# Performance work log

Hardware: AMD Instinct MI355X
Metric: run time of the kernel (lower is better)

## Reference

```python
import jax, jax.numpy as jnp
import numpy as np

K_TOP = 10
DEPTH = 1
N_RULES = 2
N_HOPS = 2
IS_REVERSED = (False, True)


def setup_inputs() -> dict:
    key = jax.random.key(0)
    ks = jax.random.split(key, 11)
    B, E, N, F = 16, 256, 1024, 2048
    return {
        'rel': jax.random.normal(ks[0], (B, E), jnp.float32),
        'arg1': jax.random.normal(ks[1], (B, E), jnp.float32),
        'arg2': jax.random.normal(ks[2], (B, E), jnp.float32),
        'fact_rel': jax.random.normal(ks[3], (B, F, E), jnp.float32),
        'fact_arg1': jax.random.normal(ks[4], (B, F, E), jnp.float32),
        'fact_arg2': jax.random.normal(ks[5], (B, F, E), jnp.float32),
        'nb_facts': jax.random.randint(ks[6], (B,), 1, F + 1),
        'entity_embeddings': jax.random.normal(ks[7], (B, N, E), jnp.float32),
        'nb_entities': jax.random.randint(ks[8], (B,), 1, N + 1),
        'W': jax.random.normal(ks[9], (N_RULES, N_HOPS, E, E), jnp.float32) / np.sqrt(E),
        'b': jnp.zeros((N_RULES, N_HOPS, E), jnp.float32),
    }


def _kernel_scores(q, f):
    # q: [B, M, E], f: [B, F, E] -> Gaussian kernel exp(-0.5*||q-f||^2): [B, M, F]
    d = (jnp.sum(q * q, -1)[..., None] + jnp.sum(f * f, -1)[:, None, :]
         - 2.0 * jnp.einsum('bme,bfe->bmf', q, f))
    return jnp.exp(-0.5 * jnp.maximum(d, 0.0))


def kb_score(rel, arg1, arg2, fact_rel, fact_arg1, fact_arg2, nb_facts):
    # BatchNeuralKB.score: product of per-component kernels, mask padded facts, max over facts.
    B, F, E = fact_rel.shape
    M = rel.shape[0] // B
    r = rel.reshape(B, M, E); a1 = arg1.reshape(B, M, E); a2 = arg2.reshape(B, M, E)
    s = (_kernel_scores(r, fact_rel) * _kernel_scores(a1, fact_arg1)
         * _kernel_scores(a2, fact_arg2))                       # [B, M, F]
    mask = jnp.arange(F)[None, None, :] < nb_facts[:, None, None]
    s = jnp.where(mask, s, 0.0)
    return jnp.max(s, axis=-1).reshape(-1)                      # [B*M]


def prove(rel, arg1, arg2, fact_rel, fact_arg1, fact_arg2, nb_facts,
          entity_embeddings, W, b, depth):
    scores_0 = kb_score(rel, arg1, arg2, fact_rel, fact_arg1, fact_arg2, nb_facts)
    if depth == 0:
        return scores_0
    B, E = rel.shape
    N = entity_embeddings.shape[1]
    global_res = None
    for rule_idx in range(N_RULES):
        is_rev = IS_REVERSED[rule_idx]
        hop_rel_lst = [rel @ W[rule_idx, h] + b[rule_idx, h] for h in range(N_HOPS)]
        sources, scores = arg1, None
        for hop_idx, hop_rel in enumerate(hop_rel_lst, start=1):
            sources_2d = sources.reshape(-1, E)
            nb_branches = sources_2d.shape[0] // B
            hop_rel_2d = jnp.repeat(hop_rel, nb_branches, axis=0)   # [B*br, E]
            if hop_idx < N_HOPS:
                ent_rep = jnp.repeat(entity_embeddings, nb_branches, axis=0)  # [B*br, N, E]
                all_ent_2d = ent_rep.reshape(-1, E)                  # [B*br*N, E]
                new_src_2d = jnp.repeat(sources_2d, N, axis=0)       # [B*br*N, E]
                hop_rel_big = jnp.repeat(hop_rel_2d, N, axis=0)
                na1, na2 = (all_ent_2d, new_src_2d) if is_rev else (new_src_2d, all_ent_2d)
                new_scores = prove(hop_rel_big, na1, na2, fact_rel, fact_arg1,
                                   fact_arg2, nb_facts, entity_embeddings, W, b,
                                   depth - 1).reshape(-1, N)         # [B*br, N]
                k = min(K_TOP, N)
                z_scores, z_idx = jax.lax.top_k(new_scores, k)       # [B*br, k]
                z_emb = jnp.take_along_axis(ent_rep, z_idx[..., None], axis=1)  # [B*br, k, E]
                sources = z_emb.reshape(-1, E)
                z1d = z_scores.reshape(-1)
                scores = z1d if scores is None else jnp.minimum(z1d, jnp.repeat(scores, k))
            else:
                arg2_2d = jnp.repeat(arg2, nb_branches, axis=0)
                na1, na2 = (arg2_2d, sources_2d) if is_rev else (sources_2d, arg2_2d)
                z1d = prove(hop_rel_2d, na1, na2, fact_rel, fact_arg1, fact_arg2,
                            nb_facts, entity_embeddings, W, b, depth - 1)
                scores = z1d if scores is None else jnp.minimum(z1d, scores)
        res = jnp.max(scores.reshape(B, -1), axis=1)
        global_res = res if global_res is None else jnp.maximum(global_res, res)
    return jnp.maximum(scores_0, global_res)


def reference(rel, arg1, arg2, fact_rel, fact_arg1, fact_arg2, nb_facts,
              entity_embeddings, nb_entities, W, b):
    return prove(rel, arg1, arg2, fact_rel, fact_arg1, fact_arg2, nb_facts,
                 entity_embeddings, W, b, depth=DEPTH)
```

## Files before the change

### kernel.cpp

```cpp
#include <hip/hip_runtime.h>
#include <math.h>

#define E 256
#define KTOP 10
#define NY 8
#define NINF (-__builtin_huge_valf())

typedef __attribute__((ext_vector_type(4))) float f32x4;
typedef __attribute__((ext_vector_type(2))) long i64x2;

__device__ inline float wsum(float v) {
    v += __shfl_xor(v, 1, 64);
    v += __shfl_xor(v, 2, 64);
    v += __shfl_xor(v, 4, 64);
    v += __shfl_xor(v, 8, 64);
    v += __shfl_xor(v, 16, 64);
    v += __shfl_xor(v, 32, 64);
    return v;
}

__device__ inline float wmax(float v) {
    v = fmaxf(v, __shfl_xor(v, 1, 64));
    v = fmaxf(v, __shfl_xor(v, 2, 64));
    v = fmaxf(v, __shfl_xor(v, 4, 64));
    v = fmaxf(v, __shfl_xor(v, 8, 64));
    v = fmaxf(v, __shfl_xor(v, 16, 64));
    v = fmaxf(v, __shfl_xor(v, 32, 64));
    return v;
}

__device__ inline float dot4(float4 a, float4 b) {
    return a.x * b.x + a.y * b.y + a.z * b.z + a.w * b.w;
}

__device__ inline void atomicMaxF(float* addr, float v) {
    atomicMax((unsigned int*)addr, __float_as_uint(v));
}

__device__ inline unsigned char f2fp8(float x) {
    unsigned u = __float_as_uint(x);
    unsigned s = (u >> 24) & 0x80u;
    int e = (int)((u >> 23) & 0xFF) - 127;
    unsigned m = u & 0x7FFFFFu;
    if (e < -9) return (unsigned char)s;
    if (e > 8) return (unsigned char)(s | 0x7E);
    if (e >= -6) {
        unsigned mant = m >> 20;
        unsigned rest = m & 0xFFFFFu;
        if (rest > 0x80000u || (rest == 0x80000u && (mant & 1))) mant++;
        unsigned v = (((unsigned)(e + 7)) << 3) + mant;
        if (v > 0x7Eu) v = 0x7Eu;
        return (unsigned char)(s | v);
    }
    int rs = 20 + (-6 - e);
    unsigned full = 0x800000u | m;
    unsigned mant = full >> rs;
    unsigned rem = full & ((1u << rs) - 1u);
    unsigned half = 1u << (rs - 1);
    if (rem > half || (rem == half && (mant & 1))) mant++;
    if (mant >= 8u) return (unsigned char)(s | 0x08u);
    return (unsigned char)(s | mant);
}

#if defined(__has_builtin)
#if __has_builtin(__builtin_amdgcn_cvt_pk_fp8_f32)
#define HAVE_HW_FP8 1
#endif
#endif

__device__ inline unsigned pack_fp8x4(float a, float b, float c, float d) {
#ifdef HAVE_HW_FP8
    int lo = __builtin_amdgcn_cvt_pk_fp8_f32(a, b, 0, false);
    return (unsigned)__builtin_amdgcn_cvt_pk_fp8_f32(c, d, lo, true);
#else
    return (unsigned)f2fp8(a) | ((unsigned)f2fp8(b) << 8) |
           ((unsigned)f2fp8(c) << 16) | ((unsigned)f2fp8(d) << 24);
#endif
}

__device__ inline int tile_off(int e0, int col) {
    return ((e0 >> 6) << 10) + (((e0 & 31) >> 3) << 8) + (col << 4) +
           (((e0 >> 5) & 1) << 3) + (e0 & 7);
}

__global__ void k_hoprel(const float* __restrict__ rel, const float* __restrict__ W,
                         const float* __restrict__ bias, float* __restrict__ hr,
                         int B) {
    int b = blockIdx.x, rh = blockIdx.y;
    int j = threadIdx.x;
    __shared__ float relS[E];
    relS[j] = rel[b * E + j];
    __syncthreads();
    const float* Wp = W + (size_t)rh * E * E;
    float acc = bias[rh * E + j];
#pragma unroll 8
    for (int e = 0; e < E; ++e) acc = fmaf(relS[e], Wp[e * E + j], acc);
    hr[((size_t)rh * B + b) * E + j] = acc;
}

__global__ void k_prep_ent(const float* __restrict__ ent, unsigned char* __restrict__ entb,
                           unsigned char* __restrict__ entt, float* __restrict__ ne_,
                           int BN, int N) {
    int row = blockIdx.x * 4 + (threadIdx.x >> 6);
    if (row >= BN) return;
    int lane = threadIdx.x & 63;
    float4 v = ((const float4*)(ent + (size_t)row * E))[lane];
    float s = wsum(dot4(v, v));
    if (lane == 0) ne_[row] = s;
    unsigned o = pack_fp8x4(v.x, v.y, v.z, v.w);
    ((unsigned*)(entb + (size_t)row * E))[lane] = o;
    int b = row / N, n = row % N;
    size_t tbase = ((size_t)b * (N >> 4) + (n >> 4)) * 4096;
    *(unsigned*)(entt + tbase + tile_off(lane * 4, n & 15)) = o;
}

__global__ __launch_bounds__(256) void k_cast(
    const float* __restrict__ frel, const float* __restrict__ fa1,
    const float* __restrict__ fa2, unsigned char* __restrict__ frb,
    unsigned char* __restrict__ fa1b, unsigned char* __restrict__ fa2b,
    int B, int F) {
    int row = blockIdx.x * 4 + (threadIdx.x >> 6);
    int lane = threadIdx.x & 63;
    int BF = B * F;
    if (row >= 3 * BF) return;
    int a = row / BF, rem = row - a * BF;
    int b = rem / F, f = rem - b * F;
    const float* src = (a == 0) ? frel : (a == 1) ? fa1 : fa2;
    unsigned char* dst = (a == 0) ? frb : (a == 1) ? fa1b : fa2b;
    float4 v = ((const float4*)(src + (size_t)rem * E))[lane];
    size_t tbase = ((size_t)b * (F >> 4) + (f >> 4)) * 4096;
    *(unsigned*)(dst + tbase + tile_off(lane * 4, f & 15)) =
        pack_fp8x4(v.x, v.y, v.z, v.w);
}

__global__ __launch_bounds__(64) void k_prep_q(
    const float* __restrict__ rel, const float* __restrict__ arg1,
    const float* __restrict__ arg2, const float* __restrict__ hr,
    unsigned char* __restrict__ qt, int B) {
    int b = blockIdx.x;
    int lane = threadIdx.x;
    unsigned char* t = qt + (size_t)b * 4096;
#define ROW(q, ptr)                                                       \
    {                                                                     \
        float4 v = ((const float4*)(ptr))[lane];                          \
        *(unsigned*)(t + tile_off(lane * 4, q)) =                         \
            pack_fp8x4(v.x, v.y, v.z, v.w);                               \
    }
    ROW(0, rel + (size_t)b * E)
    ROW(1, arg1 + (size_t)b * E)
    ROW(2, arg2 + (size_t)b * E)
    ROW(3, hr + ((size_t)0 * B + b) * E)
    ROW(4, hr + ((size_t)1 * B + b) * E)
    ROW(5, hr + ((size_t)2 * B + b) * E)
    ROW(6, hr + ((size_t)3 * B + b) * E)
#undef ROW
#pragma unroll
    for (int q = 7; q < 16; ++q)
        *(unsigned*)(t + tile_off(lane * 4, q)) = 0u;
}

__global__ __launch_bounds__(256) void k_pair(
    const unsigned char* __restrict__ qt, const unsigned char* __restrict__ frb,
    const unsigned char* __restrict__ fa1b, const unsigned char* __restrict__ fa2b,
    const int* __restrict__ nbf, float* __restrict__ lw1, float* __restrict__ lw2,
    float* __restrict__ s0log, float* __restrict__ nf1, float* __restrict__ nf2,
    int B, int F) {
    int b = blockIdx.y;
    int lane = threadIdx.x & 63, wave = threadIdx.x >> 6;
    int ti = blockIdx.x * 4 + wave;
    int f0 = ti * 16;
    int lr = lane & 15, lk = lane >> 4;
    const unsigned char* qp = qt + (size_t)b * 4096 + lk * 256 + lr * 16;
    size_t tb = ((size_t)b * (F >> 4) + ti) * 4096;
    const unsigned char* frp = frb + tb + lk * 256 + lr * 16;
    const unsigned char* f1p = fa1b + tb + lk * 256 + lr * 16;
    const unsigned char* f2p = fa2b + tb + lk * 256 + lr * 16;
    long Q[8], FR[8], F1[8], F2[8];
#pragma unroll
    for (int g = 0; g < 4; ++g) {
        i64x2 a = *(const i64x2*)(qp + g * 1024);
        Q[2 * g] = a.x; Q[2 * g + 1] = a.y;
        i64x2 c = *(const i64x2*)(frp + g * 1024);
        FR[2 * g] = c.x; FR[2 * g + 1] = c.y;
        i64x2 d = *(const i64x2*)(f1p + g * 1024);
        F1[2 * g] = d.x; F1[2 * g + 1] = d.y;
        i64x2 e2 = *(const i64x2*)(f2p + g * 1024);
        F2[2 * g] = e2.x; F2[2 * g + 1] = e2.y;
    }
    f32x4 Dqq = {0.f, 0.f, 0.f, 0.f}, D1 = Dqq, D2 = Dqq, D3 = Dqq, D4 = Dqq,
          D5 = Dqq, D6 = Dqq;
#pragma unroll
    for (int kb = 0; kb < 8; ++kb) {
        Dqq = __builtin_amdgcn_mfma_f32_16x16x32_fp8_fp8(Q[kb], Q[kb], Dqq, 0, 0, 0);
        D1 = __builtin_amdgcn_mfma_f32_16x16x32_fp8_fp8(Q[kb], FR[kb], D1, 0, 0, 0);
        D2 = __builtin_amdgcn_mfma_f32_16x16x32_fp8_fp8(Q[kb], F1[kb], D2, 0, 0, 0);
        D3 = __builtin_amdgcn_mfma_f32_16x16x32_fp8_fp8(Q[kb], F2[kb], D3, 0, 0, 0);
        D4 = __builtin_amdgcn_mfma_f32_16x16x32_fp8_fp8(FR[kb], FR[kb], D4, 0, 0, 0);
        D5 = __builtin_amdgcn_mfma_f32_16x16x32_fp8_fp8(F1[kb], F1[kb], D5, 0, 0, 0);
        D6 = __builtin_amdgcn_mfma_f32_16x16x32_fp8_fp8(F2[kb], F2[kb], D6, 0, 0, 0);
    }
    __shared__ float vals[4][16][12];
    __shared__ float qn[4][8];
#pragma unroll
    for (int j = 0; j < 4; ++j) {
        int q = lk * 4 + j;
        if (q == 0) vals[wave][lr][0] = D1[j];
        if (q == 3) vals[wave][lr][1] = D1[j];
        if (q == 4) vals[wave][lr][2] = D1[j];
        if (q == 5) vals[wave][lr][3] = D1[j];
        if (q == 6) vals[wave][lr][4] = D1[j];
        if (q == 1) { vals[wave][lr][5] = D2[j]; vals[wave][lr][7] = D3[j]; }
        if (q == 2) { vals[wave][lr][6] = D2[j]; vals[wave][lr][8] = D3[j]; }
        if (q == lr) {
            vals[wave][lr][9] = D4[j];
            vals[wave][lr][10] = D5[j];
            vals[wave][lr][11] = D6[j];
            if (q < 7) qn[wave][q] = Dqq[j];
        }
    }
    if (lane < 16) {
        int f = f0 + lane;
        size_t bf = (size_t)b * F + f;
        const float* vv = vals[wave][lane];
        float nfr = vv[9], n1 = vv[10], n2 = vv[11];
        bool msk = (f < nbf[b]);
        float rrel  = fmaxf(qn[wave][0] + nfr - 2.f * vv[0], 0.f);
        float rh00  = fmaxf(qn[wave][3] + nfr - 2.f * vv[1], 0.f);
        float rh01  = fmaxf(qn[wave][4] + nfr - 2.f * vv[2], 0.f);
        float rh10  = fmaxf(qn[wave][5] + nfr - 2.f * vv[3], 0.f);
        float rh11  = fmaxf(qn[wave][6] + nfr - 2.f * vv[4], 0.f);
        float ra1f1 = fmaxf(qn[wave][1] + n1 - 2.f * vv[5], 0.f);
        float ra2f1 = fmaxf(qn[wave][2] + n1 - 2.f * vv[6], 0.f);
        float ra1f2 = fmaxf(qn[wave][1] + n2 - 2.f * vv[7], 0.f);
        float ra2f2 = fmaxf(qn[wave][2] + n2 - 2.f * vv[8], 0.f);
        nf1[bf] = n1;
        nf2[bf] = n2;
        lw1[bf]                 = msk ? -0.5f * (rh00 + ra1f1) : NINF;
        lw1[(size_t)B * F + bf] = msk ? -0.5f * (rh10 + ra1f2) : NINF;
        lw2[bf]                 = msk ? -0.5f * (rh01 + ra2f2) : NINF;
        lw2[(size_t)B * F + bf] = msk ? -0.5f * (rh11 + ra2f1) : NINF;
        s0log[bf] = msk ? -0.5f * (rrel + ra1f1 + ra2f2) : NINF;
    }
}

__global__ void k_s0red(const float* __restrict__ s0log, float* __restrict__ out,
                        int B, int F) {
    int b = blockIdx.x;
    int tid = threadIdx.x, lane = tid & 63, wave = tid >> 6;
    float m = NINF;
    for (int f = tid; f < F; f += 256) m = fmaxf(m, s0log[(size_t)b * F + f]);
    m = wmax(m);
    __shared__ float red[4];
    if (lane == 0) red[wave] = m;
    __syncthreads();
    if (tid == 0) out[b] = expf(fmaxf(fmaxf(red[0], red[1]), fmaxf(red[2], red[3])));
}

__global__ __launch_bounds__(256, 4) void k_hop1m(
    const unsigned char* __restrict__ entt, const unsigned char* __restrict__ fa1b,
    const unsigned char* __restrict__ fa2b, const float* __restrict__ nf1,
    const float* __restrict__ nf2, const float* __restrict__ ne,
    const float* __restrict__ lw1, float* __restrict__ nsc_part, int B, int N, int F) {
    int L = blockIdx.x;
    int xcd = L & 7, s = L >> 3;
    int b = ((s >> 7) << 3) | xcd;
    int inner = s & 127;
    int r = inner >> 6, nb = (inner >> 3) & 7, fs = inner & 7;
    int BR = nb * 128;
    int F0 = fs * 256;
    const unsigned char* factb = (r == 0) ? fa2b : fa1b;
    const float* nfp = ((r == 0) ? nf2 : nf1) + (size_t)b * F;
    const float* w = lw1 + ((size_t)r * B + b) * F;
    const float* nep = ne + (size_t)b * N;

    __shared__ unsigned char bT[2][4096];

    int tid = threadIdx.x, lane = tid & 63, wave = tid >> 6;
    int lr = lane & 15, lk = lane >> 4;
    int row0 = BR + wave * 32;

    const unsigned char* At = entt + (size_t)b * N * E;
    long areg[2][8];
#pragma unroll
    for (int m = 0; m < 2; ++m) {
        const unsigned char* p = At + (size_t)((row0 >> 4) + m) * 4096 + lk * 256 +
                                 lr * 16;
#pragma unroll
        for (int g = 0; g < 4; ++g) {
            i64x2 vv = *(const i64x2*)(p + g * 1024);
            areg[m][2 * g] = vv.x;
            areg[m][2 * g + 1] = vv.y;
        }
    }
    float nh[2][4];
#pragma unroll
    for (int m = 0; m < 2; ++m)
#pragma unroll
        for (int j = 0; j < 4; ++j)
            nh[m][j] = -0.5f * nep[row0 + m * 16 + lk * 4 + j];
    float lwa[16], gfa[16];
#pragma unroll
    for (int t = 0; t < 16; ++t) {
        int fcol = F0 + t * 16 + lr;
        lwa[t] = w[fcol];
        gfa[t] = fmaf(-0.5f, nfp[fcol], lwa[t]);
    }
    float vmax[2][4];
#pragma unroll
    for (int m = 0; m < 2; ++m)
#pragma unroll
        for (int j = 0; j < 4; ++j) vmax[m][j] = NINF;

    const unsigned char* Bt = factb + (size_t)b * F * E + (size_t)(F0 >> 4) * 4096;
#define STG(buf, t)                                                            \
    __builtin_amdgcn_global_load_lds(                                          \
        (const __attribute__((address_space(1))) void*)(Bt + (size_t)(t) * 4096 + \
                                                        wave * 1024 + lane * 16), \
        (__attribute__((address_space(3))) void*)&bT[buf][wave * 1024], 16, 0, 0)

    STG(0, 0);
    __syncthreads();
#pragma unroll
    for (int t = 0; t < 16; ++t) {
        int cur = t & 1;
        if (t < 15) STG(cur ^ 1, t + 1);
        long bfr[8];
#pragma unroll
        for (int g = 0; g < 4; ++g) {
            i64x2 vv = *(const i64x2*)&bT[cur][g * 1024 + lane * 16];
            bfr[2 * g] = vv.x;
            bfr[2 * g + 1] = vv.y;
        }
        f32x4 acc0 = {0.f, 0.f, 0.f, 0.f}, acc1 = {0.f, 0.f, 0.f, 0.f};
#pragma unroll
        for (int kb = 0; kb < 8; ++kb) {
            acc0 = __builtin_amdgcn_mfma_f32_16x16x32_fp8_fp8(areg[0][kb], bfr[kb],
                                                              acc0, 0, 0, 0);
            acc1 = __builtin_amdgcn_mfma_f32_16x16x32_fp8_fp8(areg[1][kb], bfr[kb],
                                                              acc1, 0, 0, 0);
        }
#pragma unroll
        for (int j = 0; j < 4; ++j) {
            vmax[0][j] = fmaxf(vmax[0][j], fminf(acc0[j] + gfa[t] + nh[0][j], lwa[t]));
            vmax[1][j] = fmaxf(vmax[1][j], fminf(acc1[j] + gfa[t] + nh[1][j], lwa[t]));
        }
        __syncthreads();
    }
#undef STG

#pragma unroll
    for (int m = 0; m < 2; ++m)
#pragma unroll
        for (int j = 0; j < 4; ++j) {
            float v = vmax[m][j];
            v = fmaxf(v, __shfl_xor(v, 1, 64));
            v = fmaxf(v, __shfl_xor(v, 2, 64));
            v = fmaxf(v, __shfl_xor(v, 4, 64));
            v = fmaxf(v, __shfl_xor(v, 8, 64));
            if (lr == 0) {
                int row = row0 + m * 16 + lk * 4 + j;
                nsc_part[(size_t)fs * (2 * (size_t)B * N) +
                         ((size_t)r * B + b) * N + row] = v;
            }
        }
}

__global__ __launch_bounds__(256) void k_topk(const float* __restrict__ nsc_part,
                                              float* __restrict__ zval,
                                              int* __restrict__ zidx, int B, int N) {
    int b = blockIdx.x, r = blockIdx.y;
    int tid = threadIdx.x, lane = tid & 63, wave = tid >> 6;
    size_t rbN = ((size_t)r * B + b) * N;
    size_t ystr = 2 * (size_t)B * N;
    const float4* p0 = (const float4*)(nsc_part + rbN) + tid;
    float4 m = *p0;
#pragma unroll
    for (int y = 1; y < NY; ++y) {
        float4 t = *(const float4*)((const float*)p0 + (size_t)y * ystr);
        m.x = fmaxf(m.x, t.x); m.y = fmaxf(m.y, t.y);
        m.z = fmaxf(m.z, t.z); m.w = fmaxf(m.w, t.w);
    }
    float v0 = expf(m.x), v1 = expf(m.y), v2 = expf(m.z), v3 = expf(m.w);
    int base = tid * 4;
    __shared__ float rv[4];
    __shared__ int ri[4];
    for (int t = 0; t < KTOP; ++t) {
        float bv = v0; int bi = base;
        if (v1 > bv) { bv = v1; bi = base + 1; }
        if (v2 > bv) { bv = v2; bi = base + 2; }
        if (v3 > bv) { bv = v3; bi = base + 3; }
#pragma unroll
        for (int off = 32; off > 0; off >>= 1) {
            float ov = __shfl_xor(bv, off, 64);
            int oi = __shfl_xor(bi, off, 64);
            if (ov > bv || (ov == bv && oi < bi)) { bv = ov; bi = oi; }
        }
        if (lane == 0) { rv[wave] = bv; ri[wave] = bi; }
        __syncthreads();
        float fb = rv[0]; int fi = ri[0];
#pragma unroll
        for (int wv = 1; wv < 4; ++wv) {
            float ov = rv[wv]; int oi = ri[wv];
            if (ov > fb || (ov == fb && oi < fi)) { fb = ov; fi = oi; }
        }
        if (tid == 0) {
            zval[((size_t)r * B + b) * KTOP + t] = fb;
            zidx[((size_t)r * B + b) * KTOP + t] = fi;
        }
        int off = fi - base;
        v0 = (off == 0) ? -2.f : v0;
        v1 = (off == 1) ? -2.f : v1;
        v2 = (off == 2) ? -2.f : v2;
        v3 = (off == 3) ? -2.f : v3;
        __syncthreads();
    }
}

__global__ __launch_bounds__(256) void k_hop2m(
    const unsigned char* __restrict__ entb, const unsigned char* __restrict__ fa1b,
    const unsigned char* __restrict__ fa2b, const float* __restrict__ nf1,
    const float* __restrict__ nf2, const float* __restrict__ ne,
    const float* __restrict__ lw2, const int* __restrict__ zidx,
    float* __restrict__ h2part, int B, int N, int F) {
    int L = blockIdx.x;
    int xcd = L & 7, s = L >> 3;
    int b = ((s >> 4) << 3) | xcd;
    int inner = s & 15;
    int r = inner >> 3, c = inner & 7;
    const unsigned char* factb = (r == 0) ? fa1b : fa2b;
    const float* nfp = ((r == 0) ? nf1 : nf2) + (size_t)b * F;
    const float* w = lw2 + ((size_t)r * B + b) * F;
    int tid = threadIdx.x, lane = tid & 63, wave = tid >> 6;
    int lr = lane & 15, lk = lane >> 4;
    __shared__ unsigned char aLds[32 * 16 * 8];
    __shared__ float snrm[16];
    for (int ci = tid; ci < 512; ci += 256) {
        int row = ci & 15, kc = ci >> 4;
        long vv = 0;
        if (row < KTOP) {
            int idx = zidx[((size_t)r * B + b) * KTOP + row];
            vv = *(const long*)(entb + ((size_t)b * N + idx) * E + kc * 8);
        }
        *(long*)&aLds[(size_t)ci * 8] = vv;
    }
    if (tid < 16) {
        float nv = 0.f;
        if (tid < KTOP) {
            int idx = zidx[((size_t)r * B + b) * KTOP + tid];
            nv = ne[(size_t)b * N + idx];
        }
        snrm[tid] = nv;
    }
    __syncthreads();
    long afr[8];
#pragma unroll
    for (int kb = 0; kb < 8; ++kb)
        afr[kb] = *(const long*)&aLds[((kb * 4 + lk) * 16 + lr) * 8];
    float nhs[4];
#pragma unroll
    for (int j = 0; j < 4; ++j) nhs[j] = -0.5f * snrm[lk * 4 + j];
    int fbase = c * (F >> 3) + wave * (F >> 5);
    float vmax[4] = {NINF, NINF, NINF, NINF};
    const unsigned char* Bb = factb + (size_t)b * F * E;
#pragma unroll
    for (int n = 0; n < 4; ++n) {
        int fcol = fbase + n * 16;
        const unsigned char* p = Bb + (size_t)(fcol >> 4) * 4096 + lk * 256 + lr * 16;
        long bfr[8];
#pragma unroll
        for (int g = 0; g < 4; ++g) {
            i64x2 vv = *(const i64x2*)(p + g * 1024);
            bfr[2 * g] = vv.x;
            bfr[2 * g + 1] = vv.y;
        }
        f32x4 acc = {0.f, 0.f, 0.f, 0.f};
#pragma unroll
        for (int kb = 0; kb < 8; ++kb)
            acc = __builtin_amdgcn_mfma_f32_16x16x32_fp8_fp8(afr[kb], bfr[kb], acc,
                                                             0, 0, 0);
        float lwf = w[fcol + lr];
        float gf = fmaf(-0.5f, nfp[fcol + lr], lwf);
#pragma unroll
        for (int j = 0; j < 4; ++j)
            vmax[j] = fmaxf(vmax[j], fminf(acc[j] + gf + nhs[j], lwf));
    }
#pragma unroll
    for (int j = 0; j < 4; ++j) {
        float v = vmax[j];
        v = fmaxf(v, __shfl_xor(v, 1, 64));
        v = fmaxf(v, __shfl_xor(v, 2, 64));
        v = fmaxf(v, __shfl_xor(v, 4, 64));
        v = fmaxf(v, __shfl_xor(v, 8, 64));
        int sidx = lk * 4 + j;
        if (lr == 0 && sidx < KTOP)
            h2part[(((size_t)r * B + b) * KTOP + sidx) * 32 + c * 4 + wave] = v;
    }
}

__global__ void k_hop2c(const float* __restrict__ h2part, const float* __restrict__ zval,
                        float* __restrict__ out, int B) {
    int i = blockIdx.x * 256 + threadIdx.x;
    int n = 2 * B * KTOP;
    if (i < n) {
        int b = (i / KTOP) % B;
        float m = NINF;
#pragma unroll
        for (int c2 = 0; c2 < 32; ++c2) m = fmaxf(m, h2part[(size_t)i * 32 + c2]);
        float sc = fminf(expf(m), zval[i]);
        atomicMaxF(&out[b], sc);
    }
}

extern "C" void kernel_launch(void* const* d_in, const int* in_sizes, int n_in,
                              void* d_out, int out_size, void* d_ws, size_t ws_size,
                              hipStream_t stream) {
    const float* rel = (const float*)d_in[0];
    const float* arg1 = (const float*)d_in[1];
    const float* arg2 = (const float*)d_in[2];
    const float* frel = (const float*)d_in[3];
    const float* fa1 = (const float*)d_in[4];
    const float* fa2 = (const float*)d_in[5];
    const int* nbf = (const int*)d_in[6];
    const float* ent = (const float*)d_in[7];
    const float* W = (const float*)d_in[9];
    const float* bias = (const float*)d_in[10];
    int B = in_sizes[0] / E;
    int F = in_sizes[3] / (B * E);
    int N = in_sizes[7] / (B * E);
    float* out = (float*)d_out;

    float* ws = (float*)d_ws;
    size_t o = 0;
    float* hr = ws + o;   o += (size_t)4 * B * E;
    float* nf1 = ws + o;  o += (size_t)B * F;
    float* nf2 = ws + o;  o += (size_t)B * F;
    float* ne_ = ws + o;  o += (size_t)B * N;
    float* lw1 = ws + o;  o += (size_t)2 * B * F;
    float* lw2 = ws + o;  o += (size_t)2 * B * F;
    float* zval = ws + o; o += (size_t)2 * B * KTOP;
    int* zidx = (int*)(ws + o); o += (size_t)2 * B * KTOP;
    float* s0log = ws + o; o += (size_t)B * F;
    float* h2part = ws + o; o += (size_t)2 * B * KTOP * 32;
    float* nsc_part = ws + o; o += (size_t)NY * 2 * B * N;
    unsigned char* fa1b = (unsigned char*)(ws + o); o += (size_t)B * F * E / 4;
    unsigned char* fa2b = (unsigned char*)(ws + o); o += (size_t)B * F * E / 4;
    unsigned char* frb = (unsigned char*)(ws + o);  o += (size_t)B * F * E / 4;
    unsigned char* entb = (unsigned char*)(ws + o); o += (size_t)B * N * E / 4;
    unsigned char* entt = (unsigned char*)(ws + o); o += (size_t)B * N * E / 4;
    unsigned char* qt = (unsigned char*)(ws + o);   o += (size_t)B * 1024;

    k_hoprel<<<dim3(B, 4), dim3(E), 0, stream>>>(rel, W, bias, hr, B);
    k_prep_ent<<<dim3((B * N + 3) / 4), dim3(256), 0, stream>>>(ent, entb, entt, ne_,
                                                                B * N, N);
    k_cast<<<dim3((3 * B * F + 3) / 4), dim3(256), 0, stream>>>(frel, fa1, fa2, frb,
                                                                fa1b, fa2b, B, F);
    k_prep_q<<<dim3(B), dim3(64), 0, stream>>>(rel, arg1, arg2, hr, qt, B);
    k_pair<<<dim3(F / 64, B), dim3(256), 0, stream>>>(qt, frb, fa1b, fa2b, nbf, lw1,
                                                      lw2, s0log, nf1, nf2, B, F);
    k_s0red<<<dim3(B), dim3(256), 0, stream>>>(s0log, out, B, F);
    k_hop1m<<<dim3(2048), dim3(256), 0, stream>>>(entt, fa1b, fa2b, nf1, nf2, ne_, lw1,
                                                  nsc_part, B, N, F);
    k_topk<<<dim3(B, 2), dim3(256), 0, stream>>>(nsc_part, zval, zidx, B, N);
    k_hop2m<<<dim3(256), dim3(256), 0, stream>>>(entb, fa1b, fa2b, nf1, nf2, ne_, lw2,
                                                 zidx, h2part, B, N, F);
    k_hop2c<<<dim3((2 * B * KTOP + 255) / 256), dim3(256), 0, stream>>>(h2part, zval,
                                                                        out, B);
}
```

Baseline: 99.94 us.

## Fuse fact fp8 cast into pair-scoring kernel via shared-memory tiles

Merges the separate fp8 cast kernel into the pair kernel. Each block loads a 16-fact tile of all three fact tensors, packs it to fp8 in shared memory, writes out only the arg1/arg2 tiles still needed later, and runs the MFMA scoring from LDS. This removes one launch, the frb buffer, and the global write-then-read round trip of the cast data. In exchange only one of the four waves does the MFMA work, and the grid now has four times as many blocks.

After: 94.37 us. 5.6% less time.

```diff
diff --git a/kernel.cpp b/kernel.cpp
--- a/kernel.cpp
+++ b/kernel.cpp
@@ -114,25 +114,6 @@
     *(unsigned*)(entt + tbase + tile_off(lane * 4, n & 15)) = o;
 }
 
-__global__ __launch_bounds__(256) void k_cast(
-    const float* __restrict__ frel, const float* __restrict__ fa1,
-    const float* __restrict__ fa2, unsigned char* __restrict__ frb,
-    unsigned char* __restrict__ fa1b, unsigned char* __restrict__ fa2b,
-    int B, int F) {
-    int row = blockIdx.x * 4 + (threadIdx.x >> 6);
-    int lane = threadIdx.x & 63;
-    int BF = B * F;
-    if (row >= 3 * BF) return;
-    int a = row / BF, rem = row - a * BF;
-    int b = rem / F, f = rem - b * F;
-    const float* src = (a == 0) ? frel : (a == 1) ? fa1 : fa2;
-    unsigned char* dst = (a == 0) ? frb : (a == 1) ? fa1b : fa2b;
-    float4 v = ((const float4*)(src + (size_t)rem * E))[lane];
-    size_t tbase = ((size_t)b * (F >> 4) + (f >> 4)) * 4096;
-    *(unsigned*)(dst + tbase + tile_off(lane * 4, f & 15)) =
-        pack_fp8x4(v.x, v.y, v.z, v.w);
-}
-
 __global__ __launch_bounds__(64) void k_prep_q(
     const float* __restrict__ rel, const float* __restrict__ arg1,
     const float* __restrict__ arg2, const float* __restrict__ hr,
@@ -159,32 +140,50 @@
         *(unsigned*)(t + tile_off(lane * 4, q)) = 0u;
 }
 
-__global__ __launch_bounds__(256) void k_pair(
-    const unsigned char* __restrict__ qt, const unsigned char* __restrict__ frb,
-    const unsigned char* __restrict__ fa1b, const unsigned char* __restrict__ fa2b,
+__global__ __launch_bounds__(256) void k_castpair(
+    const float* __restrict__ frel, const float* __restrict__ fa1,
+    const float* __restrict__ fa2, const unsigned char* __restrict__ qt,
     const int* __restrict__ nbf, float* __restrict__ lw1, float* __restrict__ lw2,
     float* __restrict__ s0log, float* __restrict__ nf1, float* __restrict__ nf2,
+    unsigned char* __restrict__ fa1b, unsigned char* __restrict__ fa2b,
     int B, int F) {
-    int b = blockIdx.y;
-    int lane = threadIdx.x & 63, wave = threadIdx.x >> 6;
-    int ti = blockIdx.x * 4 + wave;
+    int ti = blockIdx.x, b = blockIdx.y;
     int f0 = ti * 16;
-    int lr = lane & 15, lk = lane >> 4;
-    const unsigned char* qp = qt + (size_t)b * 4096 + lk * 256 + lr * 16;
+    int tid = threadIdx.x;
+    __shared__ unsigned char sFR[4096], sF1[4096], sF2[4096];
+    __shared__ float vals[16][12];
+    __shared__ float qn[8];
+    int row = tid >> 4;
+    int cb = (tid & 15) * 4;
+    size_t rbase = ((size_t)b * F + f0 + row) * E;
+#pragma unroll
+    for (int p = 0; p < 4; ++p) {
+        int e0 = p * 64 + cb;
+        float4 vr = *(const float4*)(frel + rbase + e0);
+        float4 v1 = *(const float4*)(fa1 + rbase + e0);
+        float4 v2 = *(const float4*)(fa2 + rbase + e0);
+        int off = tile_off(e0, row);
+        *(unsigned*)&sFR[off] = pack_fp8x4(vr.x, vr.y, vr.z, vr.w);
+        *(unsigned*)&sF1[off] = pack_fp8x4(v1.x, v1.y, v1.z, v1.w);
+        *(unsigned*)&sF2[off] = pack_fp8x4(v2.x, v2.y, v2.z, v2.w);
+    }
+    __syncthreads();
     size_t tb = ((size_t)b * (F >> 4) + ti) * 4096;
-    const unsigned char* frp = frb + tb + lk * 256 + lr * 16;
-    const unsigned char* f1p = fa1b + tb + lk * 256 + lr * 16;
-    const unsigned char* f2p = fa2b + tb + lk * 256 + lr * 16;
+    *(i64x2*)(fa1b + tb + tid * 16) = *(const i64x2*)&sF1[tid * 16];
+    *(i64x2*)(fa2b + tb + tid * 16) = *(const i64x2*)&sF2[tid * 16];
+    if (tid >= 64) return;
+    int lane = tid, lr = lane & 15, lk = lane >> 4;
+    const unsigned char* qp = qt + (size_t)b * 4096 + lane * 16;
     long Q[8], FR[8], F1[8], F2[8];
 #pragma unroll
     for (int g = 0; g < 4; ++g) {
         i64x2 a = *(const i64x2*)(qp + g * 1024);
         Q[2 * g] = a.x; Q[2 * g + 1] = a.y;
-        i64x2 c = *(const i64x2*)(frp + g * 1024);
+        i64x2 c = *(const i64x2*)&sFR[g * 1024 + lane * 16];
         FR[2 * g] = c.x; FR[2 * g + 1] = c.y;
-        i64x2 d = *(const i64x2*)(f1p + g * 1024);
+        i64x2 d = *(const i64x2*)&sF1[g * 1024 + lane * 16];
         F1[2 * g] = d.x; F1[2 * g + 1] = d.y;
-        i64x2 e2 = *(const i64x2*)(f2p + g * 1024);
+        i64x2 e2 = *(const i64x2*)&sF2[g * 1024 + lane * 16];
         F2[2 * g] = e2.x; F2[2 * g + 1] = e2.y;
     }
     f32x4 Dqq = {0.f, 0.f, 0.f, 0.f}, D1 = Dqq, D2 = Dqq, D3 = Dqq, D4 = Dqq,
@@ -199,40 +198,38 @@
         D5 = __builtin_amdgcn_mfma_f32_16x16x32_fp8_fp8(F1[kb], F1[kb], D5, 0, 0, 0);
         D6 = __builtin_amdgcn_mfma_f32_16x16x32_fp8_fp8(F2[kb], F2[kb], D6, 0, 0, 0);
     }
-    __shared__ float vals[4][16][12];
-    __shared__ float qn[4][8];
 #pragma unroll
     for (int j = 0; j < 4; ++j) {
         int q = lk * 4 + j;
-        if (q == 0) vals[wave][lr][0] = D1[j];
-        if (q == 3) vals[wave][lr][1] = D1[j];
-        if (q == 4) vals[wave][lr][2] = D1[j];
-        if (q == 5) vals[wave][lr][3] = D1[j];
-        if (q == 6) vals[wave][lr][4] = D1[j];
-        if (q == 1) { vals[wave][lr][5] = D2[j]; vals[wave][lr][7] = D3[j]; }
-        if (q == 2) { vals[wave][lr][6] = D2[j]; vals[wave][lr][8] = D3[j]; }
+        if (q == 0) vals[lr][0] = D1[j];
+        if (q == 3) vals[lr][1] = D1[j];
+        if (q == 4) vals[lr][2] = D1[j];
+        if (q == 5) vals[lr][3] = D1[j];
+        if (q == 6) vals[lr][4] = D1[j];
+        if (q == 1) { vals[lr][5] = D2[j]; vals[lr][7] = D3[j]; }
+        if (q == 2) { vals[lr][6] = D2[j]; vals[lr][8] = D3[j]; }
         if (q == lr) {
-            vals[wave][lr][9] = D4[j];
-            vals[wave][lr][10] = D5[j];
-            vals[wave][lr][11] = D6[j];
-            if (q < 7) qn[wave][q] = Dqq[j];
+            vals[lr][9] = D4[j];
+            vals[lr][10] = D5[j];
+            vals[lr][11] = D6[j];
+            if (q < 7) qn[q] = Dqq[j];
         }
     }
     if (lane < 16) {
         int f = f0 + lane;
         size_t bf = (size_t)b * F + f;
-        const float* vv = vals[wave][lane];
+        const float* vv = vals[lane];
         float nfr = vv[9], n1 = vv[10], n2 = vv[11];
         bool msk = (f < nbf[b]);
-        float rrel  = fmaxf(qn[wave][0] + nfr - 2.f * vv[0], 0.f);
-        float rh00  = fmaxf(qn[wave][3] + nfr - 2.f * vv[1], 0.f);
-        float rh01  = fmaxf(qn[wave][4] + nfr - 2.f * vv[2], 0.f);
-        float rh10  = fmaxf(qn[wave][5] + nfr - 2.f * vv[3], 0.f);
-        float rh11  = fmaxf(qn[wave][6] + nfr - 2.f * vv[4], 0.f);
-        float ra1f1 = fmaxf(qn[wave][1] + n1 - 2.f * vv[5], 0.f);
-        float ra2f1 = fmaxf(qn[wave][2] + n1 - 2.f * vv[6], 0.f);
-        float ra1f2 = fmaxf(qn[wave][1] + n2 - 2.f * vv[7], 0.f);
-        float ra2f2 = fmaxf(qn[wave][2] + n2 - 2.f * vv[8], 0.f);
+        float rrel  = fmaxf(qn[0] + nfr - 2.f * vv[0], 0.f);
+        float rh00  = fmaxf(qn[3] + nfr - 2.f * vv[1], 0.f);
+        float rh01  = fmaxf(qn[4] + nfr - 2.f * vv[2], 0.f);
+        float rh10  = fmaxf(qn[5] + nfr - 2.f * vv[3], 0.f);
+        float rh11  = fmaxf(qn[6] + nfr - 2.f * vv[4], 0.f);
+        float ra1f1 = fmaxf(qn[1] + n1 - 2.f * vv[5], 0.f);
+        float ra2f1 = fmaxf(qn[2] + n1 - 2.f * vv[6], 0.f);
+        float ra1f2 = fmaxf(qn[1] + n2 - 2.f * vv[7], 0.f);
+        float ra2f2 = fmaxf(qn[2] + n2 - 2.f * vv[8], 0.f);
         nf1[bf] = n1;
         nf2[bf] = n2;
         lw1[bf]                 = msk ? -0.5f * (rh00 + ra1f1) : NINF;
@@ -544,7 +541,6 @@
     float* nsc_part = ws + o; o += (size_t)NY * 2 * B * N;
     unsigned char* fa1b = (unsigned char*)(ws + o); o += (size_t)B * F * E / 4;
     unsigned char* fa2b = (unsigned char*)(ws + o); o += (size_t)B * F * E / 4;
-    unsigned char* frb = (unsigned char*)(ws + o);  o += (size_t)B * F * E / 4;
     unsigned char* entb = (unsigned char*)(ws + o); o += (size_t)B * N * E / 4;
     unsigned char* entt = (unsigned char*)(ws + o); o += (size_t)B * N * E / 4;
     unsigned char* qt = (unsigned char*)(ws + o);   o += (size_t)B * 1024;
@@ -552,11 +548,9 @@
     k_hoprel<<<dim3(B, 4), dim3(E), 0, stream>>>(rel, W, bias, hr, B);
     k_prep_ent<<<dim3((B * N + 3) / 4), dim3(256), 0, stream>>>(ent, entb, entt, ne_,
                                                                 B * N, N);
-    k_cast<<<dim3((3 * B * F + 3) / 4), dim3(256), 0, stream>>>(frel, fa1, fa2, frb,
-                                                                fa1b, fa2b, B, F);
     k_prep_q<<<dim3(B), dim3(64), 0, stream>>>(rel, arg1, arg2, hr, qt, B);
-    k_pair<<<dim3(F / 64, B), dim3(256), 0, stream>>>(qt, frb, fa1b, fa2b, nbf, lw1,
-                                                      lw2, s0log, nf1, nf2, B, F);
+    k_castpair<<<dim3(F / 16, B), dim3(256), 0, stream>>>(
+        frel, fa1, fa2, qt, nbf, lw1, lw2, s0log, nf1, nf2, fa1b, fa2b, B, F);
     k_s0red<<<dim3(B), dim3(256), 0, stream>>>(s0log, out, B, F);
     k_hop1m<<<dim3(2048), dim3(256), 0, stream>>>(entt, fa1b, fa2b, nf1, nf2, ne_, lw1,
                                                   nsc_part, B, N, F);
```
